# Optimization experiments

Hardware: AMD Instinct MI355X
Metric: run time of the kernel (lower is better)

Reference implementation:

```python
import jax, jax.numpy as jnp
import numpy as np

B, S, D, H = 8, 1024, 1024, 16
HD = D // H
EPS = 1e-06


def setup_inputs() -> dict:
    key = jax.random.key(0)
    ks = jax.random.split(key, 10)
    sc = 0.02
    inp = {
        "y": jax.random.normal(ks[0], (B, S, D), dtype=jnp.float32),
        "y_mask": jax.random.randint(ks[1], (B, 1, 1, S), 0, 2) == 1,
        "Wq": jax.random.normal(ks[2], (D, D), dtype=jnp.float32) * sc,
        "bq": jnp.zeros((D,), jnp.float32),
        "Wk": jax.random.normal(ks[3], (D, D), dtype=jnp.float32) * sc,
        "bk": jnp.zeros((D,), jnp.float32),
        "Wv": jax.random.normal(ks[4], (D, D), dtype=jnp.float32) * sc,
        "bv": jnp.zeros((D,), jnp.float32),
        "Wm": jax.random.normal(ks[5], (D, D), dtype=jnp.float32) * sc,
        "bm": jnp.zeros((D,), jnp.float32),
        "a2": jnp.ones((D,), jnp.float32),
        "b2": jnp.zeros((D,), jnp.float32),
    }
    return inp


def _heads(x):
    # [B,S,D] -> [B,H,S,HD]
    return x.reshape(B, S, H, HD).transpose(0, 2, 1, 3)


def reference(y, y_mask, Wq, bq, Wk, bk, Wv, bv, Wm, bm, a2, b2):
    # torch Linear: x @ W^T + b
    q = _heads(y @ Wq.T + bq)
    k = _heads(y @ Wk.T + bk)
    v = _heads(y @ Wv.T + bv)
    scores = jnp.einsum("bhqd,bhkd->bhqk", q, k) / jnp.sqrt(jnp.float32(HD))
    scores = jnp.where(y_mask, jnp.float32(-1e9), scores)
    att = jax.nn.softmax(scores, axis=-1)  # dropout = identity in eval
    atted = jnp.einsum("bhqk,bhkd->bhqd", att, v)
    atted = atted.transpose(0, 2, 1, 3).reshape(B, S, D)
    atted = atted @ Wm.T + bm
    x = y + atted  # residual (dropout1 = identity in eval)
    mean = x.mean(-1, keepdims=True)
    # torch std: unbiased (ddof=1); eps added to std, not variance
    std = jnp.sqrt(((x - mean) ** 2).sum(-1, keepdims=True) / jnp.float32(D - 1))
    return a2 * (x - mean) / (std + EPS) + b2
```

## Files before the change

### kernel.cpp

```cpp
#include <hip/hip_runtime.h>

#define DEVFN __device__ __forceinline__

typedef unsigned short u16;
typedef __attribute__((ext_vector_type(8))) unsigned short u16x8;
typedef __attribute__((ext_vector_type(4))) unsigned short u16x4;
typedef __attribute__((ext_vector_type(8))) __bf16 bf16x8;
typedef __attribute__((ext_vector_type(4))) float f32x4;

DEVFN u16 f2bf_hw(float f) {
    return __builtin_bit_cast(u16, (__bf16)f);
}

DEVFN float bf2f(u16 h) {
    unsigned u = (unsigned)h << 16;
    return __builtin_bit_cast(float, u);
}

DEVFN bf16x8 ldfrag(const u16* p) {
    return __builtin_bit_cast(bf16x8, *(const u16x8*)p);
}

DEVFN f32x4 mfma16(bf16x8 a, bf16x8 b, f32x4 c) {
    return __builtin_amdgcn_mfma_f32_16x16x32_bf16(a, b, c, 0, 0, 0);
}

DEVFN void async16(const u16* g, u16* l) {
    __builtin_amdgcn_global_load_lds(
        (const __attribute__((address_space(1))) void*)g,
        (__attribute__((address_space(3))) void*)l, 16, 0, 0);
}

__global__ __launch_bounds__(256) void conv_all(const float* __restrict__ y,
                                                const float* __restrict__ w0,
                                                const float* __restrict__ w1,
                                                const float* __restrict__ w2,
                                                const float* __restrict__ w3,
                                                u16* __restrict__ yb,
                                                u16* __restrict__ wb,
                                                const int* __restrict__ mask,
                                                int* __restrict__ idx,
                                                int* __restrict__ cnt) {
    const int b = blockIdx.x;
    if (b >= 12288) {
        const int wave = threadIdx.x >> 6, lane = threadIdx.x & 63;
        for (int bb = wave; bb < 8; bb += 4) {
            const int* m = mask + bb * 1024;
            int* ib = idx + bb * 1024;
            int base = 0;
            for (int t = 0; t < 16; ++t) {
                const int pos = t * 64 + lane;
                const int valid = (m[pos] == 0) ? 1 : 0;
                const unsigned long long bal = __ballot(valid);
                const int pre = __popcll(bal & ((1ull << lane) - 1ull));
                if (valid) ib[base + pre] = pos;
                base += (int)__popcll(bal);
            }
            if (lane == 0) cnt[bb] = base;
            for (int i = base + lane; i < 1024; i += 64) ib[i] = 0;
        }
        return;
    }
    const float* src;
    u16* dst;
    int i;
    if (b < 8192) {
        src = y; dst = yb;
        i = b * 1024 + threadIdx.x * 4;
    } else {
        const int g = (b - 8192) >> 10;
        src = g == 0 ? w0 : (g == 1 ? w1 : (g == 2 ? w2 : w3));
        dst = wb + (size_t)g * 1024 * 1024;
        i = ((b - 8192) & 1023) * 1024 + threadIdx.x * 4;
    }
    const float4 v = *(const float4*)&src[i];
    u16x4 o;
    o.x = f2bf_hw(v.x); o.y = f2bf_hw(v.y);
    o.z = f2bf_hw(v.z); o.w = f2bf_hw(v.w);
    *(u16x4*)&dst[i] = o;
}

__global__ __launch_bounds__(512, 2) void gemm8b(const u16* __restrict__ A,
                                                 const u16* __restrict__ Bt,
                                                 const float* __restrict__ b0,
                                                 const float* __restrict__ b1,
                                                 const float* __restrict__ b2,
                                                 u16* __restrict__ C0,
                                                 u16* __restrict__ C1,
                                                 u16* __restrict__ C2,
                                                 int K, int NBX) {
    __shared__ u16 lds[2][24576];
    const int NT = K >> 6;
    const int tid = threadIdx.x;
    const int wave = tid >> 6, lane = tid & 63;
    const int quad = lane >> 4, l16 = lane & 15;
    const int wm = wave >> 1, wn = wave & 1;
    const int nwg = gridDim.x, cpx = nwg >> 3;
    const int sb = (blockIdx.x & 7) * cpx + (blockIdx.x >> 3);
    const int bx = sb % NBX, by = sb / NBX;
    const int m0 = by * 256, n0 = bx * 128;
    const int sr = lane >> 3, sc = lane & 7;
    const int scs = (sc ^ sr) << 3;
    const u16* Ag = A + (size_t)(m0 + wave * 8 + sr) * K + scs;
    const u16* Bg = Bt + (size_t)(n0 + wave * 8 + sr) * K + scs;
    const size_t rstep = (size_t)64 * K;
    const int swz = (quad ^ (l16 & 7)) << 3;
    const int rofA = (wm * 64 + l16) * 64 + swz;
    const int rofB = (wn * 64 + l16) * 64 + swz;

#define STAGE(gp, lp)                                        \
    do {                                                     \
        async16((gp), (lp) + wave * 512);                    \
        async16((gp) + rstep, (lp) + 4096 + wave * 512);     \
    } while (0)

    f32x4 acc[4][4] = {};

    STAGE(Ag, &lds[0][0]);
    STAGE(Ag + 2 * rstep, &lds[0][8192]);
    STAGE(Bg, &lds[0][16384]);
    STAGE(Ag + 64, &lds[1][0]);
    STAGE(Ag + 2 * rstep + 64, &lds[1][8192]);
    asm volatile("s_waitcnt vmcnt(4)" ::: "memory");
    __builtin_amdgcn_s_barrier();

    for (int t = 0; t < NT; ++t) {
        const int buf = t & 1;
        const u16* Ar = &lds[buf][0];
        const u16* Br = &lds[buf][16384];
        bf16x8 af[4][2], bfr[4][2];
        #pragma unroll
        for (int mi = 0; mi < 4; ++mi) {
            af[mi][0] = ldfrag(Ar + mi * 1024 + rofA);
            af[mi][1] = ldfrag(Ar + mi * 1024 + (rofA ^ 32));
        }
        #pragma unroll
        for (int ni = 0; ni < 2; ++ni) {
            bfr[ni][0] = ldfrag(Br + ni * 1024 + rofB);
            bfr[ni][1] = ldfrag(Br + ni * 1024 + (rofB ^ 32));
        }
        if (t + 1 < NT) STAGE(Bg + (t + 1) * 64, &lds[buf ^ 1][16384]);
        __builtin_amdgcn_s_barrier();
        asm volatile("s_waitcnt lgkmcnt(0)" ::: "memory");
        __builtin_amdgcn_s_setprio(1);
        #pragma unroll
        for (int mi = 0; mi < 4; ++mi)
            #pragma unroll
            for (int ni = 0; ni < 2; ++ni) {
                acc[mi][ni] = mfma16(af[mi][0], bfr[ni][0], acc[mi][ni]);
                acc[mi][ni] = mfma16(af[mi][1], bfr[ni][1], acc[mi][ni]);
            }
        __builtin_amdgcn_s_setprio(0);
        __builtin_amdgcn_s_barrier();
        #pragma unroll
        for (int ni = 2; ni < 4; ++ni) {
            bfr[ni][0] = ldfrag(Br + ni * 1024 + rofB);
            bfr[ni][1] = ldfrag(Br + ni * 1024 + (rofB ^ 32));
        }
        if (t + 2 < NT) {
            STAGE(Ag + (t + 2) * 64, &lds[buf][0]);
            STAGE(Ag + 2 * rstep + (t + 2) * 64, &lds[buf][8192]);
        }
        __builtin_amdgcn_s_barrier();
        asm volatile("s_waitcnt lgkmcnt(0)" ::: "memory");
        __builtin_amdgcn_s_setprio(1);
        #pragma unroll
        for (int mi = 0; mi < 4; ++mi)
            #pragma unroll
            for (int ni = 2; ni < 4; ++ni) {
                acc[mi][ni] = mfma16(af[mi][0], bfr[ni][0], acc[mi][ni]);
                acc[mi][ni] = mfma16(af[mi][1], bfr[ni][1], acc[mi][ni]);
            }
        __builtin_amdgcn_s_setprio(0);
        if (t < NT - 2)
            asm volatile("s_waitcnt vmcnt(4)" ::: "memory");
        else
            asm volatile("s_waitcnt vmcnt(0)" ::: "memory");
        __builtin_amdgcn_s_barrier();
    }
#undef STAGE
    const int wrow = m0 + wm * 64 + quad * 4;
    #pragma unroll
    for (int ni = 0; ni < 4; ++ni) {
        const int col = n0 + wn * 64 + ni * 16 + l16;
        const int cs = col >> 10;
        const int c = col & 1023;
        const float* bp = cs == 0 ? b0 : (cs == 1 ? b1 : b2);
        u16* cp = cs == 0 ? C0 : (cs == 1 ? C1 : C2);
        const float bb = bp[c];
        #pragma unroll
        for (int mi = 0; mi < 4; ++mi)
            #pragma unroll
            for (int r = 0; r < 4; ++r) {
                const int row = wrow + mi * 16 + r;
                cp[(size_t)row * 1024 + c] = f2bf_hw(acc[mi][ni][r] + bb);
            }
    }
}

__global__ __launch_bounds__(256) void attn(const u16* __restrict__ qb,
                                            const u16* __restrict__ kb,
                                            const u16* __restrict__ vb,
                                            const int* __restrict__ idxb,
                                            const int* __restrict__ cntb,
                                            u16* __restrict__ attb) {
    const int lin = blockIdx.x;
    const int xcd = lin & 7, slot = lin >> 3;
    const int bh = xcd * 16 + (slot >> 3);
    const int q0 = (slot & 7) * 128;
    const int bb = bh >> 4, h = bh & 15;
    const int tid = threadIdx.x, wave = tid >> 6, lane = tid & 63;
    const int quad = lane >> 4, l16 = lane & 15;
    __shared__ u16 lK[64 * 72];
    __shared__ u16 lV[64 * 72];
    __shared__ u16 lP[128 * 72];

    const int cn = cntb[bb];
    const int kEnd = (cn + 63) & ~63;
    const int* ib = idxb + bb * 1024;

    bf16x8 aq[2][2];
    #pragma unroll
    for (int rg = 0; rg < 2; ++rg) {
        const int qrow = q0 + wave * 32 + rg * 16 + l16;
        const u16* qp = qb + (size_t)(bb * 1024 + qrow) * 1024 + h * 64 + quad * 8;
        aq[rg][0] = ldfrag(qp);
        aq[rg][1] = ldfrag(qp + 32);
    }

    f32x4 o[2][4] = {};
    float ps_acc[2][4] = {};

    const int srow = tid >> 3, scol = (tid & 7) * 8;
    const u16* kbase = kb + (size_t)(bb * 1024) * 1024 + h * 64 + scol;
    const u16* vbase = vb + (size_t)(bb * 1024) * 1024 + h * 64 + scol;

    int gi0 = ib[srow], gi1 = ib[srow + 32];
    u16x8 nk0 = *(const u16x8*)(kbase + (size_t)gi0 * 1024);
    u16x8 nk1 = *(const u16x8*)(kbase + (size_t)gi1 * 1024);
    u16x8 nv0 = *(const u16x8*)(vbase + (size_t)gi0 * 1024);
    u16x8 nv1 = *(const u16x8*)(vbase + (size_t)gi1 * 1024);

    const float C = 0.18033688011112043f;

    for (int kt = 0; kt < kEnd; kt += 64) {
        __syncthreads();
        *(u16x8*)&lK[srow * 72 + scol] = nk0;
        *(u16x8*)&lK[(srow + 32) * 72 + scol] = nk1;
        #pragma unroll
        for (int j = 0; j < 8; ++j) {
            lV[(scol + j) * 72 + srow] = nv0[j];
            lV[(scol + j) * 72 + srow + 32] = nv1[j];
        }
        __syncthreads();
        const int ktn = kt + 64;
        if (ktn < kEnd) {
            gi0 = ib[ktn + srow]; gi1 = ib[ktn + srow + 32];
            nk0 = *(const u16x8*)(kbase + (size_t)gi0 * 1024);
            nk1 = *(const u16x8*)(kbase + (size_t)gi1 * 1024);
            nv0 = *(const u16x8*)(vbase + (size_t)gi0 * 1024);
            nv1 = *(const u16x8*)(vbase + (size_t)gi1 * 1024);
        }

        bf16x8 kf[4][2];
        #pragma unroll
        for (int n = 0; n < 4; ++n) {
            kf[n][0] = ldfrag(&lK[(n * 16 + l16) * 72 + quad * 8]);
            kf[n][1] = ldfrag(&lK[(n * 16 + l16) * 72 + 32 + quad * 8]);
        }
        f32x4 s[2][4];
        #pragma unroll
        for (int rg = 0; rg < 2; ++rg)
            #pragma unroll
            for (int n = 0; n < 4; ++n) {
                f32x4 t = {};
                t = mfma16(aq[rg][0], kf[n][0], t);
                t = mfma16(aq[rg][1], kf[n][1], t);
                s[rg][n] = t;
            }
        float bias[4];
        #pragma unroll
        for (int n = 0; n < 4; ++n)
            bias[n] = (kt + n * 16 + l16 < cn) ? 0.0f : -1e9f;
        #pragma unroll
        for (int rg = 0; rg < 2; ++rg)
            #pragma unroll
            for (int n = 0; n < 4; ++n)
                #pragma unroll
                for (int r = 0; r < 4; ++r) {
                    const float p =
                        __builtin_amdgcn_exp2f(__builtin_fmaf(s[rg][n][r], C, bias[n]));
                    ps_acc[rg][r] += p;
                    lP[(wave * 32 + rg * 16 + quad * 4 + r) * 72 + n * 16 + l16] =
                        f2bf_hw(p);
                }
        __asm__ __volatile__("s_waitcnt lgkmcnt(0)" ::: "memory");
        bf16x8 ap[2][2];
        #pragma unroll
        for (int rg = 0; rg < 2; ++rg) {
            ap[rg][0] = ldfrag(&lP[(wave * 32 + rg * 16 + l16) * 72 + quad * 8]);
            ap[rg][1] = ldfrag(&lP[(wave * 32 + rg * 16 + l16) * 72 + 32 + quad * 8]);
        }
        bf16x8 vf[4][2];
        #pragma unroll
        for (int ni = 0; ni < 4; ++ni) {
            vf[ni][0] = ldfrag(&lV[(ni * 16 + l16) * 72 + quad * 8]);
            vf[ni][1] = ldfrag(&lV[(ni * 16 + l16) * 72 + 32 + quad * 8]);
        }
        #pragma unroll
        for (int rg = 0; rg < 2; ++rg)
            #pragma unroll
            for (int ni = 0; ni < 4; ++ni) {
                o[rg][ni] = mfma16(ap[rg][0], vf[ni][0], o[rg][ni]);
                o[rg][ni] = mfma16(ap[rg][1], vf[ni][1], o[rg][ni]);
            }
    }
    #pragma unroll
    for (int off = 1; off < 16; off <<= 1)
        #pragma unroll
        for (int rg = 0; rg < 2; ++rg)
            #pragma unroll
            for (int r = 0; r < 4; ++r)
                ps_acc[rg][r] += __shfl_xor(ps_acc[rg][r], off);
    float rl[2][4];
    #pragma unroll
    for (int rg = 0; rg < 2; ++rg)
        #pragma unroll
        for (int r = 0; r < 4; ++r) rl[rg][r] = 1.f / ps_acc[rg][r];
    #pragma unroll
    for (int rg = 0; rg < 2; ++rg)
        #pragma unroll
        for (int ni = 0; ni < 4; ++ni)
            #pragma unroll
            for (int r = 0; r < 4; ++r) {
                const int row = q0 + wave * 32 + rg * 16 + quad * 4 + r;
                attb[(size_t)(bb * 1024 + row) * 1024 + h * 64 + ni * 16 + l16] =
                    f2bf_hw(o[rg][ni][r] * rl[rg][r]);
            }
}

__global__ __launch_bounds__(256) void ln_res(const u16* __restrict__ ybf,
                                              const u16* __restrict__ xpb,
                                              const float* __restrict__ a2,
                                              const float* __restrict__ b2,
                                              float* __restrict__ out) {
    const int row = blockIdx.x, tid = threadIdx.x;
    const size_t base = (size_t)row * 1024;
    const int j = tid * 4;
    const u16x4 yv = *(const u16x4*)&ybf[base + j];
    const u16x4 xv = *(const u16x4*)&xpb[base + j];
    float x[4] = {bf2f(yv.x) + bf2f(xv.x), bf2f(yv.y) + bf2f(xv.y),
                  bf2f(yv.z) + bf2f(xv.z), bf2f(yv.w) + bf2f(xv.w)};
    float s = 0.f, ss = 0.f;
    #pragma unroll
    for (int i = 0; i < 4; ++i) { s += x[i]; ss += x[i] * x[i]; }
    #pragma unroll
    for (int off = 1; off < 64; off <<= 1) {
        s += __shfl_xor(s, off);
        ss += __shfl_xor(ss, off);
    }
    __shared__ float rs[4], rss[4];
    const int wave = tid >> 6, lane = tid & 63;
    if (lane == 0) { rs[wave] = s; rss[wave] = ss; }
    __syncthreads();
    s = rs[0] + rs[1] + rs[2] + rs[3];
    ss = rss[0] + rss[1] + rss[2] + rss[3];
    const float mean = s * (1.f / 1024.f);
    float var = (ss - s * mean) * (1.f / 1023.f);
    var = fmaxf(var, 0.f);
    const float inv = 1.f / (sqrtf(var) + 1e-6f);
    const float4 av = *(const float4*)&a2[j];
    const float4 bv = *(const float4*)&b2[j];
    float4 ov;
    ov.x = av.x * (x[0] - mean) * inv + bv.x;
    ov.y = av.y * (x[1] - mean) * inv + bv.y;
    ov.z = av.z * (x[2] - mean) * inv + bv.z;
    ov.w = av.w * (x[3] - mean) * inv + bv.w;
    *(float4*)&out[base + j] = ov;
}

extern "C" void kernel_launch(void* const* d_in, const int* in_sizes, int n_in,
                              void* d_out, int out_size, void* d_ws, size_t ws_size,
                              hipStream_t stream) {
    (void)in_sizes; (void)n_in; (void)out_size;
    const float* y   = (const float*)d_in[0];
    const int*   msk = (const int*)d_in[1];
    const float* Wq  = (const float*)d_in[2];
    const float* bq  = (const float*)d_in[3];
    const float* Wk  = (const float*)d_in[4];
    const float* bkb = (const float*)d_in[5];
    const float* Wv  = (const float*)d_in[6];
    const float* bv  = (const float*)d_in[7];
    const float* Wm  = (const float*)d_in[8];
    const float* bm  = (const float*)d_in[9];
    const float* a2  = (const float*)d_in[10];
    const float* b2  = (const float*)d_in[11];
    float* out = (float*)d_out;

    char* ws = (char*)d_ws;
    const size_t MB = 1u << 20;
    if (ws_size < 72 * MB) return;
    u16* yb  = (u16*)(ws);
    u16* wqb = (u16*)(ws + 16 * MB);
    u16* wmb = (u16*)(ws + 22 * MB);
    u16* qb  = (u16*)(ws + 24 * MB);
    u16* kb  = (u16*)(ws + 40 * MB);
    u16* vb  = (u16*)(ws + 56 * MB);
    u16* xpb  = qb;

    int* idxb = (int*)d_out;
    int* cntb = idxb + 8192;
    u16* attb = (u16*)((char*)d_out + 16 * MB);

    conv_all<<<12289, 256, 0, stream>>>(y, Wq, Wk, Wv, Wm, yb, wqb,
                                        msk, idxb, cntb);

    gemm8b<<<dim3(768), 512, 0, stream>>>(
        yb, wqb, bq, bkb, bv, qb, kb, vb, 1024, 24);

    attn<<<dim3(1024), 256, 0, stream>>>(qb, kb, vb, idxb, cntb, attb);

    gemm8b<<<dim3(256), 512, 0, stream>>>(
        attb, wmb, bm, bm, bm, xpb, xpb, xpb, 1024, 8);

    ln_res<<<8192, 256, 0, stream>>>(yb, xpb, a2, b2, out);
}
```

Before: 272.4 us.

## Add 256x256-tile QKV GEMM with interleaved staged loads and MFMA phases

Adds a new GEMM kernel, gemm9, for the fused QKV projection. It uses 256x256 output tiles instead of the previous tile shape, so the grid drops from 768 to 384 workgroups. The main loop is split into four MFMA phases, with LDS fragment reads and asynchronous global-to-LDS stages interleaved between barriers, and s_setprio is raised around the MFMA blocks. The aim is more data reuse per tile and better overlap of loads with compute. In exchange it uses more accumulator registers, adds more barriers, and with fewer workgroups risks uneven use of the CUs.

After: 275.8 us. About the same (+1.2%).

```diff
diff --git a/kernel.cpp b/kernel.cpp
--- a/kernel.cpp
+++ b/kernel.cpp
@@ -78,6 +78,158 @@
     o.x = f2bf_hw(v.x); o.y = f2bf_hw(v.y);
     o.z = f2bf_hw(v.z); o.w = f2bf_hw(v.w);
     *(u16x4*)&dst[i] = o;
+}
+
+__global__ __launch_bounds__(512, 2) void gemm9(const u16* __restrict__ A,
+                                                const u16* __restrict__ Bt,
+                                                const float* __restrict__ b0,
+                                                const float* __restrict__ b1,
+                                                const float* __restrict__ b2,
+                                                u16* __restrict__ C0,
+                                                u16* __restrict__ C1,
+                                                u16* __restrict__ C2,
+                                                int K, int NBX) {
+    __shared__ u16 lds[2][2][2][8192];
+    const int NT = K >> 6;
+    const int tid = threadIdx.x;
+    const int wave = tid >> 6, lane = tid & 63;
+    const int quad = lane >> 4, l16 = lane & 15;
+    const int wr = wave >> 2;
+    const int wc = wave & 3;
+    const int nwg = gridDim.x, cpx = nwg >> 3;
+    const int sb = (blockIdx.x & 7) * cpx + (blockIdx.x >> 3);
+    const int bx = sb % NBX, by = sb / NBX;
+    const int m0 = by * 256, n0 = bx * 256;
+    const int sr = lane >> 3, sc = lane & 7;
+    const int scs = (sc ^ sr) << 3;
+    const u16* Ag = A + (size_t)(m0 + wave * 8 + sr) * K + scs;
+    const u16* Bg = Bt + (size_t)(n0 + wave * 8 + sr) * K + scs;
+    const size_t h64 = (size_t)64 * K;
+    const int swz = (quad ^ (l16 & 7)) << 3;
+    const int brow = (wc & 1) * 64;
+
+#define STAGE(gp, lp)                                      \
+    do {                                                   \
+        async16((gp), (lp) + wave * 512);                  \
+        async16((gp) + h64, (lp) + 4096 + wave * 512);     \
+    } while (0)
+#define RD_A(dst, bf, mi)                                                     \
+    do {                                                                      \
+        dst[0] = ldfrag(&lds[bf][0][wr][((mi) * 16 + l16) * 64 + swz]);       \
+        dst[1] = ldfrag(&lds[bf][0][wr][((mi) * 16 + l16) * 64 + (swz ^ 32)]);\
+    } while (0)
+#define RD_B(dst, bf, ni)                                                         \
+    do {                                                                          \
+        dst[0] = ldfrag(&lds[bf][1][wc >> 1][(brow + (ni) * 16 + l16) * 64 + swz]);\
+        dst[1] = ldfrag(                                                          \
+            &lds[bf][1][wc >> 1][(brow + (ni) * 16 + l16) * 64 + (swz ^ 32)]);    \
+    } while (0)
+
+    f32x4 acc[8][4] = {};
+    bf16x8 afE[4][2], afL[4][2], bfr[4][2];
+
+    STAGE(Ag, &lds[0][0][0][0]);
+    STAGE(Ag + 2 * h64, &lds[0][0][1][0]);
+    STAGE(Bg, &lds[0][1][0][0]);
+    STAGE(Bg + 2 * h64, &lds[0][1][1][0]);
+    STAGE(Bg + 64, &lds[1][1][0][0]);
+    STAGE(Bg + 2 * h64 + 64, &lds[1][1][1][0]);
+    STAGE(Ag + 64, &lds[1][0][0][0]);
+    asm volatile("s_waitcnt vmcnt(6)" ::: "memory");
+    __builtin_amdgcn_s_barrier();
+    #pragma unroll
+    for (int mi = 0; mi < 4; ++mi) RD_A(afE[mi], 0, mi);
+    #pragma unroll
+    for (int ni = 0; ni < 2; ++ni) RD_B(bfr[ni], 0, ni);
+
+    for (int t = 0; t < NT; ++t) {
+        const int buf = t & 1;
+        #pragma unroll
+        for (int ni = 2; ni < 4; ++ni) RD_B(bfr[ni], buf, ni);
+        if (t + 1 < NT)
+            STAGE(Ag + 2 * h64 + (size_t)(t + 1) * 64, &lds[buf ^ 1][0][1][0]);
+        __builtin_amdgcn_s_barrier();
+        __builtin_amdgcn_s_setprio(1);
+        #pragma unroll
+        for (int mi = 0; mi < 4; ++mi)
+            #pragma unroll
+            for (int ni = 0; ni < 2; ++ni) {
+                acc[mi][ni] = mfma16(afE[mi][0], bfr[ni][0], acc[mi][ni]);
+                acc[mi][ni] = mfma16(afE[mi][1], bfr[ni][1], acc[mi][ni]);
+            }
+        __builtin_amdgcn_s_setprio(0);
+        __builtin_amdgcn_s_barrier();
+        #pragma unroll
+        for (int mi = 0; mi < 4; ++mi) RD_A(afL[mi], buf, mi + 4);
+        __builtin_amdgcn_s_barrier();
+        __builtin_amdgcn_s_setprio(1);
+        #pragma unroll
+        for (int mi = 0; mi < 4; ++mi)
+            #pragma unroll
+            for (int ni = 2; ni < 4; ++ni) {
+                acc[mi][ni] = mfma16(afE[mi][0], bfr[ni][0], acc[mi][ni]);
+                acc[mi][ni] = mfma16(afE[mi][1], bfr[ni][1], acc[mi][ni]);
+            }
+        __builtin_amdgcn_s_setprio(0);
+        __builtin_amdgcn_s_barrier();
+        if (t + 2 < NT) STAGE(Bg + (size_t)(t + 2) * 64, &lds[buf][1][0][0]);
+        __builtin_amdgcn_s_barrier();
+        __builtin_amdgcn_s_setprio(1);
+        #pragma unroll
+        for (int mi = 0; mi < 4; ++mi)
+            #pragma unroll
+            for (int ni = 0; ni < 2; ++ni) {
+                acc[mi + 4][ni] = mfma16(afL[mi][0], bfr[ni][0], acc[mi + 4][ni]);
+                acc[mi + 4][ni] = mfma16(afL[mi][1], bfr[ni][1], acc[mi + 4][ni]);
+            }
+        __builtin_amdgcn_s_setprio(0);
+        if (t < NT - 2)
+            asm volatile("s_waitcnt vmcnt(2)" ::: "memory");
+        else
+            asm volatile("s_waitcnt vmcnt(0)" ::: "memory");
+        __builtin_amdgcn_s_barrier();
+        if (t + 1 < NT) {
+            #pragma unroll
+            for (int mi = 0; mi < 4; ++mi) RD_A(afE[mi], buf ^ 1, mi);
+            #pragma unroll
+            for (int ni = 0; ni < 2; ++ni) RD_B(bfr[ni], buf ^ 1, ni);
+        }
+        if (t + 2 < NT) {
+            STAGE(Bg + 2 * h64 + (size_t)(t + 2) * 64, &lds[buf][1][1][0]);
+            STAGE(Ag + (size_t)(t + 2) * 64, &lds[buf][0][0][0]);
+        }
+        __builtin_amdgcn_s_barrier();
+        __builtin_amdgcn_s_setprio(1);
+        #pragma unroll
+        for (int mi = 0; mi < 4; ++mi)
+            #pragma unroll
+            for (int ni = 2; ni < 4; ++ni) {
+                acc[mi + 4][ni] = mfma16(afL[mi][0], bfr[ni][0], acc[mi + 4][ni]);
+                acc[mi + 4][ni] = mfma16(afL[mi][1], bfr[ni][1], acc[mi + 4][ni]);
+            }
+        __builtin_amdgcn_s_setprio(0);
+        __builtin_amdgcn_s_barrier();
+    }
+#undef STAGE
+#undef RD_A
+#undef RD_B
+    const int wrow = m0 + wr * 128 + quad * 4;
+    #pragma unroll
+    for (int ni = 0; ni < 4; ++ni) {
+        const int col = n0 + wc * 64 + ni * 16 + l16;
+        const int cs = col >> 10;
+        const int c = col & 1023;
+        const float* bp = cs == 0 ? b0 : (cs == 1 ? b1 : b2);
+        u16* cp = cs == 0 ? C0 : (cs == 1 ? C1 : C2);
+        const float bb = bp[c];
+        #pragma unroll
+        for (int mi = 0; mi < 8; ++mi)
+            #pragma unroll
+            for (int r = 0; r < 4; ++r) {
+                const int row = wrow + mi * 16 + r;
+                cp[(size_t)row * 1024 + c] = f2bf_hw(acc[mi][ni][r] + bb);
+            }
+    }
 }
 
 __global__ __launch_bounds__(512, 2) void gemm8b(const u16* __restrict__ A,
@@ -415,8 +567,8 @@
     conv_all<<<12289, 256, 0, stream>>>(y, Wq, Wk, Wv, Wm, yb, wqb,
                                         msk, idxb, cntb);
 
-    gemm8b<<<dim3(768), 512, 0, stream>>>(
-        yb, wqb, bq, bkb, bv, qb, kb, vb, 1024, 24);
+    gemm9<<<dim3(384), 512, 0, stream>>>(
+        yb, wqb, bq, bkb, bv, qb, kb, vb, 1024, 12);
 
     attn<<<dim3(1024), 256, 0, stream>>>(qb, kb, vb, idxb, cntb, attb);
 
```

## Compute K/V projections only for unmasked keys, compacted via index list

Applied to the files above, without the earlier changes.

Adds a dedicated QKV GEMM kernel. The Q projection stays dense, but the K/V projections gather only the key rows that survive the mask (via idxb) and write them compacted. M-tiles beyond the padded valid count exit early. Attention then reads K/V contiguously instead of through indirect gathered loads. This cuts GEMM FLOPs for masked-out keys and removes the index indirection in attention, at the cost of gathered A-row loads in the GEMM and some load imbalance across blocks that exit early.

After: 265.7 us. 1.03x faster.

```diff
diff --git a/kernel.cpp b/kernel.cpp
--- a/kernel.cpp
+++ b/kernel.cpp
@@ -78,6 +78,156 @@
     o.x = f2bf_hw(v.x); o.y = f2bf_hw(v.y);
     o.z = f2bf_hw(v.z); o.w = f2bf_hw(v.w);
     *(u16x4*)&dst[i] = o;
+}
+
+__global__ __launch_bounds__(512, 2) void gemm_qkv(const u16* __restrict__ A,
+                                                   const u16* __restrict__ Wq,
+                                                   const u16* __restrict__ Wkv,
+                                                   const float* __restrict__ bq,
+                                                   const float* __restrict__ bk,
+                                                   const float* __restrict__ bv,
+                                                   u16* __restrict__ qb,
+                                                   u16* __restrict__ kb,
+                                                   u16* __restrict__ vb,
+                                                   const int* __restrict__ idxb,
+                                                   const int* __restrict__ cntb) {
+    const int K = 1024;
+    __shared__ u16 lds[2][24576];
+    const int tid = threadIdx.x;
+    const int wave = tid >> 6, lane = tid & 63;
+    const int quad = lane >> 4, l16 = lane & 15;
+    const int wm = wave >> 1, wn = wave & 1;
+    const int cpx = gridDim.x >> 3;
+    const int sb = (blockIdx.x & 7) * cpx + (blockIdx.x >> 3);
+    int m0, n0, rowbase;
+    const u16* Bt;
+    const float *bp0, *bp1;
+    u16 *cp0, *cp1;
+    const int* ib = nullptr;
+    if (sb < 256) {
+        m0 = (sb >> 3) * 256;
+        n0 = (sb & 7) * 128;
+        rowbase = 0;
+        Bt = Wq; bp0 = bq; bp1 = bq; cp0 = qb; cp1 = qb;
+    } else {
+        const int t = sb - 256;
+        const int nb = t & 15, mb = (t >> 4) & 3, b = t >> 6;
+        const int cn = cntb[b];
+        const int pc = (cn + 255) & ~255;
+        m0 = mb * 256;
+        if (m0 >= pc) return;
+        n0 = nb * 128;
+        rowbase = b * 1024;
+        ib = idxb + b * 1024;
+        Bt = Wkv; bp0 = bk; bp1 = bv; cp0 = kb; cp1 = vb;
+    }
+    const int sr = lane >> 3, sc = lane & 7;
+    const int scs = (sc ^ sr) << 3;
+    const int ar = m0 + wave * 8 + sr;
+    int r0 = ar, r1 = ar + 64, r2 = ar + 128, r3 = ar + 192;
+    if (ib) { r0 = ib[r0]; r1 = ib[r1]; r2 = ib[r2]; r3 = ib[r3]; }
+    const u16* As0 = A + (size_t)(rowbase + r0) * K + scs;
+    const u16* As1 = A + (size_t)(rowbase + r1) * K + scs;
+    const u16* As2 = A + (size_t)(rowbase + r2) * K + scs;
+    const u16* As3 = A + (size_t)(rowbase + r3) * K + scs;
+    const u16* Bs0 = Bt + (size_t)(n0 + wave * 8 + sr) * K + scs;
+    const u16* Bs1 = Bs0 + (size_t)64 * K;
+    const int swz = (quad ^ (l16 & 7)) << 3;
+    const int rofA = (wm * 64 + l16) * 64 + swz;
+    const int rofB = (wn * 64 + l16) * 64 + swz;
+
+#define STA(off, bf)                                           \
+    do {                                                       \
+        async16(As0 + (off), &lds[bf][0] + wave * 512);        \
+        async16(As1 + (off), &lds[bf][4096] + wave * 512);     \
+        async16(As2 + (off), &lds[bf][8192] + wave * 512);     \
+        async16(As3 + (off), &lds[bf][12288] + wave * 512);    \
+    } while (0)
+#define STB(off, bf)                                           \
+    do {                                                       \
+        async16(Bs0 + (off), &lds[bf][16384] + wave * 512);    \
+        async16(Bs1 + (off), &lds[bf][20480] + wave * 512);    \
+    } while (0)
+
+    f32x4 acc[4][4] = {};
+    const int NT = K >> 6;
+
+    STA(0, 0);
+    STB(0, 0);
+    STA(64, 1);
+    asm volatile("s_waitcnt vmcnt(4)" ::: "memory");
+    __builtin_amdgcn_s_barrier();
+
+    for (int t = 0; t < NT; ++t) {
+        const int buf = t & 1;
+        const u16* Ar = &lds[buf][0];
+        const u16* Br = &lds[buf][16384];
+        bf16x8 af[4][2], bfr[4][2];
+        #pragma unroll
+        for (int mi = 0; mi < 4; ++mi) {
+            af[mi][0] = ldfrag(Ar + mi * 1024 + rofA);
+            af[mi][1] = ldfrag(Ar + mi * 1024 + (rofA ^ 32));
+        }
+        #pragma unroll
+        for (int ni = 0; ni < 2; ++ni) {
+            bfr[ni][0] = ldfrag(Br + ni * 1024 + rofB);
+            bfr[ni][1] = ldfrag(Br + ni * 1024 + (rofB ^ 32));
+        }
+        if (t + 1 < NT) STB((t + 1) * 64, buf ^ 1);
+        __builtin_amdgcn_s_barrier();
+        asm volatile("s_waitcnt lgkmcnt(0)" ::: "memory");
+        __builtin_amdgcn_s_setprio(1);
+        #pragma unroll
+        for (int mi = 0; mi < 4; ++mi)
+            #pragma unroll
+            for (int ni = 0; ni < 2; ++ni) {
+                acc[mi][ni] = mfma16(af[mi][0], bfr[ni][0], acc[mi][ni]);
+                acc[mi][ni] = mfma16(af[mi][1], bfr[ni][1], acc[mi][ni]);
+            }
+        __builtin_amdgcn_s_setprio(0);
+        __builtin_amdgcn_s_barrier();
+        #pragma unroll
+        for (int ni = 2; ni < 4; ++ni) {
+            bfr[ni][0] = ldfrag(Br + ni * 1024 + rofB);
+            bfr[ni][1] = ldfrag(Br + ni * 1024 + (rofB ^ 32));
+        }
+        if (t + 2 < NT) STA((t + 2) * 64, buf);
+        __builtin_amdgcn_s_barrier();
+        asm volatile("s_waitcnt lgkmcnt(0)" ::: "memory");
+        __builtin_amdgcn_s_setprio(1);
+        #pragma unroll
+        for (int mi = 0; mi < 4; ++mi)
+            #pragma unroll
+            for (int ni = 2; ni < 4; ++ni) {
+                acc[mi][ni] = mfma16(af[mi][0], bfr[ni][0], acc[mi][ni]);
+                acc[mi][ni] = mfma16(af[mi][1], bfr[ni][1], acc[mi][ni]);
+            }
+        __builtin_amdgcn_s_setprio(0);
+        if (t < NT - 2)
+            asm volatile("s_waitcnt vmcnt(4)" ::: "memory");
+        else
+            asm volatile("s_waitcnt vmcnt(0)" ::: "memory");
+        __builtin_amdgcn_s_barrier();
+    }
+#undef STA
+#undef STB
+    const int wrow = m0 + wm * 64 + quad * 4;
+    #pragma unroll
+    for (int ni = 0; ni < 4; ++ni) {
+        const int col = n0 + wn * 64 + ni * 16 + l16;
+        const int cs = col >> 10;
+        const int c = col & 1023;
+        const float* bp = cs == 0 ? bp0 : bp1;
+        u16* cp = cs == 0 ? cp0 : cp1;
+        const float bb = bp[c];
+        #pragma unroll
+        for (int mi = 0; mi < 4; ++mi)
+            #pragma unroll
+            for (int r = 0; r < 4; ++r) {
+                const int row = rowbase + wrow + mi * 16 + r;
+                cp[(size_t)row * 1024 + c] = f2bf_hw(acc[mi][ni][r] + bb);
+            }
+    }
 }
 
 __global__ __launch_bounds__(512, 2) void gemm8b(const u16* __restrict__ A,
@@ -201,7 +351,6 @@
 __global__ __launch_bounds__(256) void attn(const u16* __restrict__ qb,
                                             const u16* __restrict__ kb,
                                             const u16* __restrict__ vb,
-                                            const int* __restrict__ idxb,
                                             const int* __restrict__ cntb,
                                             u16* __restrict__ attb) {
     const int lin = blockIdx.x;
@@ -217,7 +366,6 @@
 
     const int cn = cntb[bb];
     const int kEnd = (cn + 63) & ~63;
-    const int* ib = idxb + bb * 1024;
 
     bf16x8 aq[2][2];
     #pragma unroll
@@ -235,11 +383,10 @@
     const u16* kbase = kb + (size_t)(bb * 1024) * 1024 + h * 64 + scol;
     const u16* vbase = vb + (size_t)(bb * 1024) * 1024 + h * 64 + scol;
 
-    int gi0 = ib[srow], gi1 = ib[srow + 32];
-    u16x8 nk0 = *(const u16x8*)(kbase + (size_t)gi0 * 1024);
-    u16x8 nk1 = *(const u16x8*)(kbase + (size_t)gi1 * 1024);
-    u16x8 nv0 = *(const u16x8*)(vbase + (size_t)gi0 * 1024);
-    u16x8 nv1 = *(const u16x8*)(vbase + (size_t)gi1 * 1024);
+    u16x8 nk0 = *(const u16x8*)(kbase + (size_t)srow * 1024);
+    u16x8 nk1 = *(const u16x8*)(kbase + (size_t)(srow + 32) * 1024);
+    u16x8 nv0 = *(const u16x8*)(vbase + (size_t)srow * 1024);
+    u16x8 nv1 = *(const u16x8*)(vbase + (size_t)(srow + 32) * 1024);
 
     const float C = 0.18033688011112043f;
 
@@ -255,11 +402,10 @@
         __syncthreads();
         const int ktn = kt + 64;
         if (ktn < kEnd) {
-            gi0 = ib[ktn + srow]; gi1 = ib[ktn + srow + 32];
-            nk0 = *(const u16x8*)(kbase + (size_t)gi0 * 1024);
-            nk1 = *(const u16x8*)(kbase + (size_t)gi1 * 1024);
-            nv0 = *(const u16x8*)(vbase + (size_t)gi0 * 1024);
-            nv1 = *(const u16x8*)(vbase + (size_t)gi1 * 1024);
+            nk0 = *(const u16x8*)(kbase + (size_t)(ktn + srow) * 1024);
+            nk1 = *(const u16x8*)(kbase + (size_t)(ktn + srow + 32) * 1024);
+            nv0 = *(const u16x8*)(vbase + (size_t)(ktn + srow) * 1024);
+            nv1 = *(const u16x8*)(vbase + (size_t)(ktn + srow + 32) * 1024);
         }
 
         bf16x8 kf[4][2];
@@ -415,10 +561,10 @@
     conv_all<<<12289, 256, 0, stream>>>(y, Wq, Wk, Wv, Wm, yb, wqb,
                                         msk, idxb, cntb);
 
-    gemm8b<<<dim3(768), 512, 0, stream>>>(
-        yb, wqb, bq, bkb, bv, qb, kb, vb, 1024, 24);
-
-    attn<<<dim3(1024), 256, 0, stream>>>(qb, kb, vb, idxb, cntb, attb);
+    gemm_qkv<<<dim3(768), 512, 0, stream>>>(
+        yb, wqb, wqb + 1024 * 1024, bq, bkb, bv, qb, kb, vb, idxb, cntb);
+
+    attn<<<dim3(1024), 256, 0, stream>>>(qb, kb, vb, cntb, attb);
 
     gemm8b<<<dim3(256), 512, 0, stream>>>(
         attb, wmb, bm, bm, bm, xpb, xpb, xpb, 1024, 8);
```

## Project K/V only for unmasked rows via work-stealing compacted GEMM

Applied to the files above, without the earlier changes.

Replaces the fused QKV GEMM with a persistent work-stealing GEMM driven by an atomic counter. It computes Q for all rows but K and V only for the compacted list of unmasked key rows per batch, writing them densely so attention reads contiguous K/V instead of gathering through an index list. This cuts K/V projection FLOPs roughly in proportion to the masked fraction and removes the gather in attention. In exchange it uses a smaller 128x128 tile with single-buffered LDS and no overlap, and adds a serial offset table plus an atomic per work item.

Result: slower. 280.6 us (+3.0%).

```diff
diff --git a/kernel.cpp b/kernel.cpp
--- a/kernel.cpp
+++ b/kernel.cpp
@@ -40,9 +40,12 @@
                                                 u16* __restrict__ wb,
                                                 const int* __restrict__ mask,
                                                 int* __restrict__ idx,
-                                                int* __restrict__ cnt) {
+                                                int* __restrict__ cnt,
+                                                int* __restrict__ kvoff,
+                                                int* __restrict__ ctr) {
     const int b = blockIdx.x;
     if (b >= 12288) {
+        __shared__ int scnt[8];
         const int wave = threadIdx.x >> 6, lane = threadIdx.x & 63;
         for (int bb = wave; bb < 8; bb += 4) {
             const int* m = mask + bb * 1024;
@@ -56,8 +59,18 @@
                 if (valid) ib[base + pre] = pos;
                 base += (int)__popcll(bal);
             }
-            if (lane == 0) cnt[bb] = base;
+            if (lane == 0) { cnt[bb] = base; scnt[bb] = base; }
             for (int i = base + lane; i < 1024; i += 64) ib[i] = 0;
+        }
+        __syncthreads();
+        if (threadIdx.x == 0) {
+            int off = 0;
+            kvoff[0] = 0;
+            for (int bb = 0; bb < 8; ++bb) {
+                off += ((scnt[bb] + 127) >> 7) << 4;
+                kvoff[bb + 1] = off;
+            }
+            *ctr = 0;
         }
         return;
     }
@@ -78,6 +91,106 @@
     o.x = f2bf_hw(v.x); o.y = f2bf_hw(v.y);
     o.z = f2bf_hw(v.z); o.w = f2bf_hw(v.w);
     *(u16x4*)&dst[i] = o;
+}
+
+__global__ __launch_bounds__(256, 4) void gemm_ws(const u16* __restrict__ A,
+                                                  const u16* __restrict__ Wq,
+                                                  const u16* __restrict__ Wkv,
+                                                  const float* __restrict__ bq,
+                                                  const float* __restrict__ bk,
+                                                  const float* __restrict__ bv,
+                                                  u16* __restrict__ qb,
+                                                  u16* __restrict__ kb,
+                                                  u16* __restrict__ vb,
+                                                  const int* __restrict__ idxb,
+                                                  const int* __restrict__ kvoff,
+                                                  int* __restrict__ ctr) {
+    const int K = 1024;
+    __shared__ u16 lA[128 * 32];
+    __shared__ u16 lB[128 * 32];
+    __shared__ int s_item;
+    __shared__ int s_kv[9];
+    const int tid = threadIdx.x;
+    if (tid < 9) s_kv[tid] = kvoff[tid];
+    const int wave = tid >> 6, lane = tid & 63;
+    const int quad = lane >> 4, l16 = lane & 15;
+    const int wm = (wave >> 1) * 64, wn = (wave & 1) * 64;
+    const int srow = tid >> 2, scol = (tid & 3) * 8;
+    u16* lA0 = &lA[wave * 512];
+    u16* lA1 = &lA[2048 + wave * 512];
+    u16* lB0 = &lB[wave * 512];
+    u16* lB1 = &lB[2048 + wave * 512];
+    for (;;) {
+        if (tid == 0) s_item = atomicAdd(ctr, 1);
+        __syncthreads();
+        const int item = s_item;
+        if (item >= 512 + s_kv[8]) return;
+        int m0, n0, rowbase = 0;
+        const u16* Bt;
+        const float *bp0, *bp1;
+        u16 *cp0, *cp1;
+        const int* ib = nullptr;
+        if (item < 512) {
+            m0 = (item >> 3) * 128;
+            n0 = (item & 7) * 128;
+            Bt = Wq; bp0 = bq; bp1 = bq; cp0 = qb; cp1 = qb;
+        } else {
+            int r = item - 512;
+            int bsel = 0;
+            while (r >= s_kv[bsel + 1]) ++bsel;
+            const int local = r - s_kv[bsel];
+            m0 = (local >> 4) * 128;
+            n0 = (local & 15) * 128;
+            rowbase = bsel * 1024;
+            ib = idxb + bsel * 1024;
+            Bt = Wkv; bp0 = bk; bp1 = bv; cp0 = kb; cp1 = vb;
+        }
+        int r0 = m0 + srow, r1 = m0 + 64 + srow;
+        if (ib) { r0 = ib[r0]; r1 = ib[r1]; }
+        const u16* Ag0 = A + (size_t)(rowbase + r0) * K + scol;
+        const u16* Ag1 = A + (size_t)(rowbase + r1) * K + scol;
+        const u16* Bg0 = Bt + (size_t)(n0 + srow) * K + scol;
+        const u16* Bg1 = Bt + (size_t)(n0 + 64 + srow) * K + scol;
+        f32x4 acc[4][4] = {};
+        for (int k0 = 0; k0 < K; k0 += 32) {
+            __syncthreads();
+            async16(Ag0 + k0, lA0);
+            async16(Ag1 + k0, lA1);
+            async16(Bg0 + k0, lB0);
+            async16(Bg1 + k0, lB1);
+            __syncthreads();
+            bf16x8 af[4], bfr[4];
+            #pragma unroll
+            for (int i = 0; i < 4; ++i)
+                af[i] = ldfrag(&lA[(wm + i * 16 + l16) * 32 + quad * 8]);
+            #pragma unroll
+            for (int i = 0; i < 4; ++i)
+                bfr[i] = ldfrag(&lB[(wn + i * 16 + l16) * 32 + quad * 8]);
+            #pragma unroll
+            for (int mi = 0; mi < 4; ++mi)
+                #pragma unroll
+                for (int ni = 0; ni < 4; ++ni)
+                    acc[mi][ni] = mfma16(af[mi], bfr[ni], acc[mi][ni]);
+        }
+        #pragma unroll
+        for (int mi = 0; mi < 4; ++mi) {
+            #pragma unroll
+            for (int ni = 0; ni < 4; ++ni) {
+                const int col = n0 + wn + ni * 16 + l16;
+                const int cs = col >> 10;
+                const int c = col & 1023;
+                const float* bp = cs == 0 ? bp0 : bp1;
+                u16* cp = cs == 0 ? cp0 : cp1;
+                const float bb = bp[c];
+                #pragma unroll
+                for (int r = 0; r < 4; ++r) {
+                    const int row = m0 + wm + mi * 16 + quad * 4 + r;
+                    cp[(size_t)(rowbase + row) * 1024 + c] =
+                        f2bf_hw(acc[mi][ni][r] + bb);
+                }
+            }
+        }
+    }
 }
 
 __global__ __launch_bounds__(512, 2) void gemm8b(const u16* __restrict__ A,
@@ -201,7 +314,6 @@
 __global__ __launch_bounds__(256) void attn(const u16* __restrict__ qb,
                                             const u16* __restrict__ kb,
                                             const u16* __restrict__ vb,
-                                            const int* __restrict__ idxb,
                                             const int* __restrict__ cntb,
                                             u16* __restrict__ attb) {
     const int lin = blockIdx.x;
@@ -217,7 +329,6 @@
 
     const int cn = cntb[bb];
     const int kEnd = (cn + 63) & ~63;
-    const int* ib = idxb + bb * 1024;
 
     bf16x8 aq[2][2];
     #pragma unroll
@@ -235,11 +346,10 @@
     const u16* kbase = kb + (size_t)(bb * 1024) * 1024 + h * 64 + scol;
     const u16* vbase = vb + (size_t)(bb * 1024) * 1024 + h * 64 + scol;
 
-    int gi0 = ib[srow], gi1 = ib[srow + 32];
-    u16x8 nk0 = *(const u16x8*)(kbase + (size_t)gi0 * 1024);
-    u16x8 nk1 = *(const u16x8*)(kbase + (size_t)gi1 * 1024);
-    u16x8 nv0 = *(const u16x8*)(vbase + (size_t)gi0 * 1024);
-    u16x8 nv1 = *(const u16x8*)(vbase + (size_t)gi1 * 1024);
+    u16x8 nk0 = *(const u16x8*)(kbase + (size_t)srow * 1024);
+    u16x8 nk1 = *(const u16x8*)(kbase + (size_t)(srow + 32) * 1024);
+    u16x8 nv0 = *(const u16x8*)(vbase + (size_t)srow * 1024);
+    u16x8 nv1 = *(const u16x8*)(vbase + (size_t)(srow + 32) * 1024);
 
     const float C = 0.18033688011112043f;
 
@@ -255,11 +365,10 @@
         __syncthreads();
         const int ktn = kt + 64;
         if (ktn < kEnd) {
-            gi0 = ib[ktn + srow]; gi1 = ib[ktn + srow + 32];
-            nk0 = *(const u16x8*)(kbase + (size_t)gi0 * 1024);
-            nk1 = *(const u16x8*)(kbase + (size_t)gi1 * 1024);
-            nv0 = *(const u16x8*)(vbase + (size_t)gi0 * 1024);
-            nv1 = *(const u16x8*)(vbase + (size_t)gi1 * 1024);
+            nk0 = *(const u16x8*)(kbase + (size_t)(ktn + srow) * 1024);
+            nk1 = *(const u16x8*)(kbase + (size_t)(ktn + srow + 32) * 1024);
+            nv0 = *(const u16x8*)(vbase + (size_t)(ktn + srow) * 1024);
+            nv1 = *(const u16x8*)(vbase + (size_t)(ktn + srow + 32) * 1024);
         }
 
         bf16x8 kf[4][2];
@@ -408,17 +517,20 @@
     u16* vb  = (u16*)(ws + 56 * MB);
     u16* xpb  = qb;
 
-    int* idxb = (int*)d_out;
-    int* cntb = idxb + 8192;
+    int* idxb  = (int*)d_out;
+    int* cntb  = idxb + 8192;
+    int* kvoffb = idxb + 8200;
+    int* ctrb  = idxb + 8212;
     u16* attb = (u16*)((char*)d_out + 16 * MB);
 
     conv_all<<<12289, 256, 0, stream>>>(y, Wq, Wk, Wv, Wm, yb, wqb,
-                                        msk, idxb, cntb);
-
-    gemm8b<<<dim3(768), 512, 0, stream>>>(
-        yb, wqb, bq, bkb, bv, qb, kb, vb, 1024, 24);
-
-    attn<<<dim3(1024), 256, 0, stream>>>(qb, kb, vb, idxb, cntb, attb);
+                                        msk, idxb, cntb, kvoffb, ctrb);
+
+    gemm_ws<<<dim3(1024), 256, 0, stream>>>(
+        yb, wqb, wqb + 1024 * 1024, bq, bkb, bv, qb, kb, vb,
+        idxb, kvoffb, ctrb);
+
+    attn<<<dim3(1024), 256, 0, stream>>>(qb, kb, vb, cntb, attb);
 
     gemm8b<<<dim3(256), 512, 0, stream>>>(
         attb, wmb, bm, bm, bm, xpb, xpb, xpb, 1024, 8);
```
